# Optimization experiments

Measured on AMD Instinct MI355X. Metric: run time of the kernel, lower is better.

Reference implementation:

```python
import jax, jax.numpy as jnp
import numpy as np
import math

INPUT_SIZE = 1024
HIDDEN_SIZE = 1024
BATCH = 4096


def setup_inputs() -> dict:
    key = jax.random.key(0)
    ks = jax.random.split(key, 16)
    stddev = 1.0 / math.sqrt(HIDDEN_SIZE)

    def unif(k, shape):
        return jax.random.uniform(k, shape, minval=-stddev, maxval=stddev, dtype=jnp.float32)

    inp = {
        'x': jax.random.normal(ks[0], (BATCH, INPUT_SIZE), dtype=jnp.float32),
        'h_prev': jax.random.normal(ks[1], (BATCH, HIDDEN_SIZE), dtype=jnp.float32),
        'c_prev': jax.random.normal(ks[2], (BATCH, HIDDEN_SIZE), dtype=jnp.float32),
        'igx': unif(ks[3], (INPUT_SIZE, HIDDEN_SIZE)),
        'igu': unif(ks[4], (HIDDEN_SIZE, HIDDEN_SIZE)),
        'ib': unif(ks[5], (HIDDEN_SIZE,)),
        'fgx': unif(ks[6], (INPUT_SIZE, HIDDEN_SIZE)),
        'fgu': unif(ks[7], (HIDDEN_SIZE, HIDDEN_SIZE)),
        'fb': unif(ks[8], (HIDDEN_SIZE,)),
        'ogx': unif(ks[9], (INPUT_SIZE, HIDDEN_SIZE)),
        'ogu': unif(ks[10], (HIDDEN_SIZE, HIDDEN_SIZE)),
        'ob': unif(ks[11], (HIDDEN_SIZE,)),
        'cgx': unif(ks[12], (INPUT_SIZE, HIDDEN_SIZE)),
        'cgu': unif(ks[13], (HIDDEN_SIZE, HIDDEN_SIZE)),
        'cb': unif(ks[14], (HIDDEN_SIZE,)),
    }
    return inp


def reference(x, h_prev, c_prev, igx, igu, ib, fgx, fgu, fb, ogx, ogu, ob, cgx, cgu, cb):
    # Fuse the 8 gate matmuls into 2 GEMMs via concatenated weights.
    # Wx: [input_size, 4H], Wh: [hidden, 4H], b: [4H]; gate order i,f,o,c.
    Wx = jnp.concatenate([igx, fgx, ogx, cgx], axis=1)
    Wh = jnp.concatenate([igu, fgu, ogu, cgu], axis=1)
    b = jnp.concatenate([ib, fb, ob, cb], axis=0)
    gates = x @ Wx + h_prev @ Wh + b  # [B, 4H]
    H = c_prev.shape[-1]
    ig = jax.nn.sigmoid(gates[:, 0 * H:1 * H])
    fg = jax.nn.sigmoid(gates[:, 1 * H:2 * H])
    og = jax.nn.sigmoid(gates[:, 2 * H:3 * H])
    cc = jnp.tanh(gates[:, 3 * H:4 * H])
    c = fg * c_prev + ig * cc
    h = og * jnp.tanh(c)
    return (h, c)
```

## Files before the change

kernel.cpp:

```cpp
#include <hip/hip_runtime.h>
#include <hip/hip_bf16.h>

typedef unsigned short u16;
typedef unsigned int u32;
typedef short bf16x8 __attribute__((ext_vector_type(8)));
typedef float f32x4 __attribute__((ext_vector_type(4)));
typedef u16 u16x8 __attribute__((ext_vector_type(8)));

#define HID 1024
#define BATCH 4096
#define KTOT 2048

__device__ __forceinline__ u16 f2bf(float f) {
  u32 v = __builtin_bit_cast(u32, f);
  u32 r = (v + 0x7fffu + ((v >> 16) & 1u)) >> 16;
  return (u16)r;
}
__device__ __forceinline__ float sigmoid_fast(float x) {
  return 1.0f / (1.0f + __expf(-x));
}
__device__ __forceinline__ float tanh_fast(float x) {
  return 2.0f * sigmoid_fast(2.0f * x) - 1.0f;
}

__global__ __launch_bounds__(256) void prep_xh(
    const float* __restrict__ x, const float* __restrict__ hp,
    u16* __restrict__ xh2) {
  int s = blockIdx.x * 256 + threadIdx.x;
  int lane = s & 63, unit = s >> 6;
  int kstep = unit & 63, rowtile = unit >> 6;
  int m = lane & 15, quad = lane >> 4;
  int row = rowtile * 16 + m;
  int kg = kstep * 32 + quad * 8;
  const float* src = (kg < 1024) ? (x + (size_t)row * 1024 + kg)
                                 : (hp + (size_t)row * 1024 + (kg - 1024));
  f32x4 a = *(const f32x4*)(src);
  f32x4 b = *(const f32x4*)(src + 4);
  u16x8 v;
#pragma unroll
  for (int j = 0; j < 4; ++j) { v[j] = f2bf(a[j]); v[j + 4] = f2bf(b[j]); }
  *(u16x8*)(xh2 + (size_t)s * 8) = v;
}

__global__ __launch_bounds__(256) void prep_w(
    const float* __restrict__ igx, const float* __restrict__ fgx,
    const float* __restrict__ ogx, const float* __restrict__ cgx,
    const float* __restrict__ igu, const float* __restrict__ fgu,
    const float* __restrict__ ogu, const float* __restrict__ cgu,
    u16* __restrict__ bt) {
  __shared__ u16 lds[64 * 66];
  const float* srcs[8] = {igx, fgx, ogx, cgx, igu, fgu, ogu, cgu};
  int bid = blockIdx.x;
  int m = bid >> 8;
  int tile = bid & 255;
  int th = tile & 15, tk = tile >> 4;
  int h0 = th << 6, k0 = tk << 6;
  int g = m & 3, which = m >> 2;
  const float* W = srcs[m] + (size_t)k0 * HID + h0;

  int t = threadIdx.x;

  int r1 = t >> 4;
  int c1 = (t & 15) << 2;
#pragma unroll
  for (int p = 0; p < 4; ++p) {
    int row = (p << 4) + r1;
    f32x4 v = *(const f32x4*)(W + (size_t)row * HID + c1);
    u32 p0 = (u32)f2bf(v[0]) | ((u32)f2bf(v[1]) << 16);
    u32 p1 = (u32)f2bf(v[2]) | ((u32)f2bf(v[3]) << 16);
    u32* d = (u32*)&lds[row * 66 + c1];
    d[0] = p0;
    d[1] = p1;
  }
  __syncthreads();

  int u = t >> 5;
  int j = u & 3, ks = u >> 2;
  int s0 = (t & 31) << 1;
  int ntile = (((h0 >> 4) + j) << 2) | g;
  size_t unit = (size_t)ntile * 64 + (size_t)which * 32 + (k0 >> 5) + ks;
  u16* dst = bt + unit * 512 + (size_t)s0 * 8;
#pragma unroll
  for (int p = 0; p < 2; ++p) {
    int s = s0 + p;
    int m16 = s & 15, quad = s >> 4;
    u16x8 v;
#pragma unroll
    for (int jj = 0; jj < 8; ++jj)
      v[jj] = lds[(ks * 32 + quad * 8 + jj) * 66 + (j << 4) + m16];
    *(u16x8*)(dst + p * 8) = v;
  }
}

#define LOAD_FRAGS(buf, kstep_)                                              \
  {                                                                          \
    int _kk = (kstep_);                                                      \
    af[buf][0]  = *(const bf16x8*)(pA + (size_t)(0 * 64 + _kk) * 512);       \
    bfr[buf][0] = *(const bf16x8*)(pB + (size_t)(0 * 64 + _kk) * 512);       \
    bfr[buf][1] = *(const bf16x8*)(pB + (size_t)(1 * 64 + _kk) * 512);       \
    bfr[buf][2] = *(const bf16x8*)(pB + (size_t)(2 * 64 + _kk) * 512);       \
    bfr[buf][3] = *(const bf16x8*)(pB + (size_t)(3 * 64 + _kk) * 512);       \
    af[buf][1]  = *(const bf16x8*)(pA + (size_t)(1 * 64 + _kk) * 512);       \
    af[buf][2]  = *(const bf16x8*)(pA + (size_t)(2 * 64 + _kk) * 512);       \
    af[buf][3]  = *(const bf16x8*)(pA + (size_t)(3 * 64 + _kk) * 512);       \
  }

#define CONSUME_FRAGS(buf)                                                   \
  {                                                                          \
    _Pragma("unroll") for (int mi = 0; mi < 4; ++mi)                         \
        _Pragma("unroll") for (int ni = 0; ni < 4; ++ni)                     \
            acc[mi][ni] = __builtin_amdgcn_mfma_f32_16x16x32_bf16(           \
                af[buf][mi], bfr[buf][ni], acc[mi][ni], 0, 0, 0);            \
  }

#define SCHED_PIN()                                                          \
  __builtin_amdgcn_sched_group_barrier(0x020, 8, 0);       \
  __builtin_amdgcn_sched_group_barrier(0x008, 16, 0);

__global__ __launch_bounds__(64) void lstm_gemm(
    const u16* __restrict__ xh2, const u16* __restrict__ bt,
    const float* __restrict__ cprev,
    const float* __restrict__ ib, const float* __restrict__ fb,
    const float* __restrict__ ob, const float* __restrict__ cb,
    float* __restrict__ hout, float* __restrict__ cout) {
  int l = threadIdx.x;
  int bid = blockIdx.x;
  int bcol = ((bid & 7) << 3) | ((bid >> 3) & 7);
  int brow = bid >> 6;
  int lrow = l & 15, quad = l >> 4;

  f32x4 acc[4][4] = {};
  bf16x8 af[2][4], bfr[2][4];

  const u16* pA = xh2 + ((size_t)(brow * 4) * 64) * 512 + l * 8;
  const u16* pB = bt  + ((size_t)(bcol * 4) * 64) * 512 + l * 8;

  LOAD_FRAGS(0, 0)
  for (int kt = 0; kt < 64; kt += 2) {
    LOAD_FRAGS(1, kt + 1)
    CONSUME_FRAGS(0)
    SCHED_PIN()
    LOAD_FRAGS(0, (kt + 2) & 63)
    CONSUME_FRAGS(1)
    SCHED_PIN()
  }

  int hcol = bcol * 16 + lrow;
  float bi = ib[hcol];
  float bff = fb[hcol];
  float bo = ob[hcol];
  float bc = cb[hcol];
  int grow = brow * 64;

#pragma unroll
  for (int mi = 0; mi < 4; ++mi) {
    int row0 = grow + mi * 16 + quad * 4;
#pragma unroll
    for (int r = 0; r < 4; ++r) {
      size_t idx = (size_t)(row0 + r) * HID + hcol;
      float gi = sigmoid_fast(acc[mi][0][r] + bi);
      float gf = sigmoid_fast(acc[mi][1][r] + bff);
      float go = sigmoid_fast(acc[mi][2][r] + bo);
      float gc = tanh_fast(acc[mi][3][r] + bc);
      float cp = cprev[idx];
      float cv = gf * cp + gi * gc;
      float hv = go * tanh_fast(cv);
      hout[idx] = hv;
      cout[idx] = cv;
    }
  }
}

extern "C" void kernel_launch(void* const* d_in, const int* in_sizes, int n_in,
                              void* d_out, int out_size, void* d_ws, size_t ws_size,
                              hipStream_t stream) {
  const float* x   = (const float*)d_in[0];
  const float* hp  = (const float*)d_in[1];
  const float* cp  = (const float*)d_in[2];
  const float* igx = (const float*)d_in[3];
  const float* igu = (const float*)d_in[4];
  const float* ib  = (const float*)d_in[5];
  const float* fgx = (const float*)d_in[6];
  const float* fgu = (const float*)d_in[7];
  const float* fb  = (const float*)d_in[8];
  const float* ogx = (const float*)d_in[9];
  const float* ogu = (const float*)d_in[10];
  const float* ob  = (const float*)d_in[11];
  const float* cgx = (const float*)d_in[12];
  const float* cgu = (const float*)d_in[13];
  const float* cb  = (const float*)d_in[14];

  u16* bt  = (u16*)d_ws;
  u16* xh2 = bt + (size_t)4096 * 2048;
  float* hout = (float*)d_out;
  float* cout = hout + (size_t)BATCH * HID;

  prep_xh<<<4096, 256, 0, stream>>>(x, hp, xh2);
  prep_w<<<2048, 256, 0, stream>>>(igx, fgx, ogx, cgx, igu, fgu, ogu, cgu, bt);
  lstm_gemm<<<4096, 64, 0, stream>>>(xh2, bt, cp, ib, fb, ob, cb, hout, cout);
}
```

Before: 231.3 us.

## Reorder packed operands kstep-major and use 4-wave blocks on a 2D grid

The bf16 staging layout for activations and weights becomes kstep-major, so fragments for one k-step sit next to each other across row and column tiles, and the GEMM loop advances pointers by a fixed stride. The GEMM kernel goes from one-wave 64x64 blocks to four-wave blocks covering 128x128 on a 32x32 grid, so co-scheduled waves share A/B fragments through cache. The aim is better L2 locality and fewer blocks. Each wave still loads directly from global memory with no LDS sharing, so the reuse depends on the cache hierarchy.

```diff
diff --git a/kernel.cpp b/kernel.cpp
--- a/kernel.cpp
+++ b/kernel.cpp
@@ -10,6 +10,7 @@
 #define HID 1024
 #define BATCH 4096
 #define KTOT 2048
+#define KSTEP_ELEMS (256 * 512)
 
 __device__ __forceinline__ u16 f2bf(float f) {
   u32 v = __builtin_bit_cast(u32, f);
@@ -28,7 +29,7 @@
     u16* __restrict__ xh2) {
   int s = blockIdx.x * 256 + threadIdx.x;
   int lane = s & 63, unit = s >> 6;
-  int kstep = unit & 63, rowtile = unit >> 6;
+  int rowtile = unit & 255, kstep = unit >> 8;
   int m = lane & 15, quad = lane >> 4;
   int row = rowtile * 16 + m;
   int kg = kstep * 32 + quad * 8;
@@ -78,7 +79,7 @@
   int j = u & 3, ks = u >> 2;
   int s0 = (t & 31) << 1;
   int ntile = (((h0 >> 4) + j) << 2) | g;
-  size_t unit = (size_t)ntile * 64 + (size_t)which * 32 + (k0 >> 5) + ks;
+  size_t unit = (size_t)(which * 32 + (k0 >> 5) + ks) * 256 + ntile;
   u16* dst = bt + unit * 512 + (size_t)s0 * 8;
 #pragma unroll
   for (int p = 0; p < 2; ++p) {
@@ -92,17 +93,16 @@
   }
 }
 
-#define LOAD_FRAGS(buf, kstep_)                                              \
+#define LOADF(buf)                                                           \
   {                                                                          \
-    int _kk = (kstep_);                                                      \
-    af[buf][0]  = *(const bf16x8*)(pA + (size_t)(0 * 64 + _kk) * 512);       \
-    bfr[buf][0] = *(const bf16x8*)(pB + (size_t)(0 * 64 + _kk) * 512);       \
-    bfr[buf][1] = *(const bf16x8*)(pB + (size_t)(1 * 64 + _kk) * 512);       \
-    bfr[buf][2] = *(const bf16x8*)(pB + (size_t)(2 * 64 + _kk) * 512);       \
-    bfr[buf][3] = *(const bf16x8*)(pB + (size_t)(3 * 64 + _kk) * 512);       \
-    af[buf][1]  = *(const bf16x8*)(pA + (size_t)(1 * 64 + _kk) * 512);       \
-    af[buf][2]  = *(const bf16x8*)(pA + (size_t)(2 * 64 + _kk) * 512);       \
-    af[buf][3]  = *(const bf16x8*)(pA + (size_t)(3 * 64 + _kk) * 512);       \
+    af[buf][0]  = *(const bf16x8*)(pA + 0 * 512);                            \
+    bfr[buf][0] = *(const bf16x8*)(pB + 0 * 512);                            \
+    bfr[buf][1] = *(const bf16x8*)(pB + 1 * 512);                            \
+    bfr[buf][2] = *(const bf16x8*)(pB + 2 * 512);                            \
+    bfr[buf][3] = *(const bf16x8*)(pB + 3 * 512);                            \
+    af[buf][1]  = *(const bf16x8*)(pA + 1 * 512);                            \
+    af[buf][2]  = *(const bf16x8*)(pA + 2 * 512);                            \
+    af[buf][3]  = *(const bf16x8*)(pA + 3 * 512);                            \
   }
 
 #define CONSUME_FRAGS(buf)                                                   \
@@ -117,44 +117,53 @@
   __builtin_amdgcn_sched_group_barrier(0x020, 8, 0);       \
   __builtin_amdgcn_sched_group_barrier(0x008, 16, 0);
 
-__global__ __launch_bounds__(64) void lstm_gemm(
+__global__ __launch_bounds__(256, 3) void lstm_gemm(
     const u16* __restrict__ xh2, const u16* __restrict__ bt,
     const float* __restrict__ cprev,
     const float* __restrict__ ib, const float* __restrict__ fb,
     const float* __restrict__ ob, const float* __restrict__ cb,
     float* __restrict__ hout, float* __restrict__ cout) {
-  int l = threadIdx.x;
-  int bid = blockIdx.x;
-  int bcol = ((bid & 7) << 3) | ((bid >> 3) & 7);
-  int brow = bid >> 6;
+  int t = threadIdx.x;
+  int brow = blockIdx.x, bcol = blockIdx.y;
+  int w = t >> 6, l = t & 63;
+  int wr = (w >> 1) * 64;
   int lrow = l & 15, quad = l >> 4;
 
   f32x4 acc[4][4] = {};
   bf16x8 af[2][4], bfr[2][4];
 
-  const u16* pA = xh2 + ((size_t)(brow * 4) * 64) * 512 + l * 8;
-  const u16* pB = bt  + ((size_t)(bcol * 4) * 64) * 512 + l * 8;
-
-  LOAD_FRAGS(0, 0)
-  for (int kt = 0; kt < 64; kt += 2) {
-    LOAD_FRAGS(1, kt + 1)
+  const u16* pA = xh2 + (size_t)(brow * 8 + (w >> 1) * 4) * 512 + (size_t)l * 8;
+  const u16* pB = bt  + (size_t)(bcol * 8 + (w & 1) * 4) * 512 + (size_t)l * 8;
+
+  LOADF(0)
+  pA += KSTEP_ELEMS; pB += KSTEP_ELEMS;
+
+  for (int it = 0; it < 31; ++it) {
+    LOADF(1)
     CONSUME_FRAGS(0)
     SCHED_PIN()
-    LOAD_FRAGS(0, (kt + 2) & 63)
+    pA += KSTEP_ELEMS; pB += KSTEP_ELEMS;
+    LOADF(0)
     CONSUME_FRAGS(1)
     SCHED_PIN()
-  }
-
-  int hcol = bcol * 16 + lrow;
+    pA += KSTEP_ELEMS; pB += KSTEP_ELEMS;
+  }
+  LOADF(1)
+  CONSUME_FRAGS(0)
+  SCHED_PIN()
+  CONSUME_FRAGS(1)
+
+  int sb = bcol * 2 + (w & 1);
+  int hcol = sb * 16 + lrow;
   float bi = ib[hcol];
   float bff = fb[hcol];
   float bo = ob[hcol];
   float bc = cb[hcol];
-  int grow = brow * 64;
+  int grow = brow * 128;
 
 #pragma unroll
   for (int mi = 0; mi < 4; ++mi) {
-    int row0 = grow + mi * 16 + quad * 4;
+    int row0 = grow + wr + mi * 16 + quad * 4;
 #pragma unroll
     for (int r = 0; r < 4; ++r) {
       size_t idx = (size_t)(row0 + r) * HID + hcol;
@@ -197,5 +206,6 @@
 
   prep_xh<<<4096, 256, 0, stream>>>(x, hp, xh2);
   prep_w<<<2048, 256, 0, stream>>>(igx, fgx, ogx, cgx, igu, fgu, ogu, cgu, bt);
-  lstm_gemm<<<4096, 64, 0, stream>>>(xh2, bt, cp, ib, fb, ob, cb, hout, cout);
-}
+  lstm_gemm<<<dim3(32, 32), 256, 0, stream>>>(xh2, bt, cp, ib, fb, ob, cb,
+                                              hout, cout);
+}
```

Result: no change. 231.5 us (+0.1%).
